# Optimization experiments

Hardware: AMD Instinct MI355X
Metric: run time of the kernel (lower is better)

## Reference

```python
import jax, jax.numpy as jnp
import numpy as np

D_MODEL = 1024
HEADS = 16
HEAD_DIM = D_MODEL // HEADS
SEQ_LEN = 2048
BATCH = 2
LN_EPS = 1e-5


def _layernorm(x, gamma, beta):
    mu = jnp.mean(x, axis=-1, keepdims=True)
    var = jnp.var(x, axis=-1, keepdims=True)
    return (x - mu) * jax.lax.rsqrt(var + LN_EPS) * gamma + beta


def setup_inputs() -> dict:
    key = jax.random.key(0)
    ks = jax.random.split(key, 12)
    d, h = D_MODEL, 4 * D_MODEL
    s = lambda fan_in: 1.0 / np.sqrt(fan_in)
    return {
        "x": jax.random.normal(ks[0], (BATCH, SEQ_LEN, d), dtype=jnp.float32),
        "W_qkv": jax.random.uniform(ks[1], (d, 3 * d), minval=-s(d), maxval=s(d)),
        "b_qkv": jax.random.uniform(ks[2], (3 * d,), minval=-s(d), maxval=s(d)),
        "W1": jax.random.uniform(ks[3], (d, h), minval=-s(d), maxval=s(d)),
        "b1": jax.random.uniform(ks[4], (h,), minval=-s(d), maxval=s(d)),
        "W2": jax.random.uniform(ks[5], (h, d), minval=-s(h), maxval=s(h)),
        "b2": jax.random.uniform(ks[6], (d,), minval=-s(h), maxval=s(h)),
        "ln1_g": jnp.ones((d,), jnp.float32),
        "ln1_b": jnp.zeros((d,), jnp.float32),
        "ln2_g": jnp.ones((d,), jnp.float32),
        "ln2_b": jnp.zeros((d,), jnp.float32),
    }


def reference(x, W_qkv, b_qkv, W1, b1, W2, b2, ln1_g, ln1_b, ln2_g, ln2_b):
    B, T, C = x.shape
    # QKV projection -> [B, T, 3, H, hs] -> q,k,v each [B, H, T, hs]
    qkv = (x @ W_qkv + b_qkv).reshape(B, T, 3, HEADS, HEAD_DIM)
    qkv = jnp.transpose(qkv, (2, 0, 3, 1, 4))
    q, k, v = qkv[0], qkv[1], qkv[2]
    # Naive causal attention with full [B,H,T,T] score matrix (matches source)
    A = jnp.einsum("bhqd,bhkd->bhqk", q, k) / jnp.sqrt(jnp.float32(HEAD_DIM))
    causal = jnp.tril(jnp.ones((T, T), dtype=bool))
    A = jnp.where(causal, A, -jnp.inf)
    A = jax.nn.softmax(A, axis=-1)
    attn = jnp.einsum("bhqk,bhkd->bhqd", A, v)  # [B,H,T,hs]
    attn = jnp.transpose(attn, (0, 2, 1, 3)).reshape(B, T, C)
    # Residual + LN, FFN, residual + LN (dropout=0 / eval)
    h = _layernorm(x + attn, ln1_g, ln1_b)
    ff = jax.nn.relu(h @ W1 + b1) @ W2 + b2
    return _layernorm(h + ff, ln2_g, ln2_b)
```

## Files before the change

kernel.cpp:

```cpp
#include <hip/hip_runtime.h>

#define D_MODEL 1024
#define HEADS   16
#define HEAD_DIM 64
#define SEQ     2048
#define BATCH   2
#define ROWS    (BATCH*SEQ)
#define FFDIM   4096

typedef __attribute__((ext_vector_type(8))) short short8;
typedef __attribute__((ext_vector_type(4))) float f32x4;
typedef __attribute__((ext_vector_type(4))) unsigned short us4;

typedef const __attribute__((address_space(1))) unsigned int* gptr_t;
typedef __attribute__((address_space(3))) unsigned int* lptr_t;

__device__ __forceinline__ unsigned short f2bf(float f){
  unsigned int x = __float_as_uint(f);
  x += 0x7fffu + ((x >> 16) & 1u);
  return (unsigned short)(x >> 16);
}

__device__ __forceinline__ float wave_sum(float x){
  #pragma unroll
  for (int off = 32; off; off >>= 1) x += __shfl_xor(x, off);
  return x;
}

__global__ __launch_bounds__(256) void cast_bf16_kernel(const float* __restrict__ in,
                                                        unsigned short* __restrict__ out, int n4){
  int i = blockIdx.x * 256 + threadIdx.x;
  if (i >= n4) return;
  float4 v = *(const float4*)(in + (size_t)i * 4);
  us4 o;
  o[0] = f2bf(v.x); o[1] = f2bf(v.y); o[2] = f2bf(v.z); o[3] = f2bf(v.w);
  *(us4*)(out + (size_t)i * 4) = o;
}

__global__ __launch_bounds__(256) void transpose_cast_kernel(const float* __restrict__ in,
                                                             unsigned short* __restrict__ out,
                                                             int R, int C){
  __shared__ float tile[32][33];
  const int bc = blockIdx.x * 32, br = blockIdx.y * 32;
  const int tx = threadIdx.x & 31, ty = threadIdx.x >> 5;
  #pragma unroll
  for (int j = 0; j < 4; ++j)
    tile[ty + 8*j][tx] = in[(size_t)(br + ty + 8*j) * C + bc + tx];
  __syncthreads();
  #pragma unroll
  for (int j = 0; j < 4; ++j)
    out[(size_t)(bc + ty + 8*j) * R + br + tx] = f2bf(tile[tx][ty + 8*j]);
}

template<int EPI>
__global__ __launch_bounds__(256) void gemm_kernel(const unsigned short* __restrict__ A,
                                                   const unsigned short* __restrict__ BT,
                                                   const float* __restrict__ bias,
                                                   int M, int N, int K, int kchunk,
                                                   int gx, int gy,
                                                   float* __restrict__ outF,
                                                   unsigned short* __restrict__ qo,
                                                   unsigned short* __restrict__ ko,
                                                   unsigned short* __restrict__ vT){
  __shared__ __align__(16) unsigned short Alds[2][128 * 32];
  __shared__ __align__(16) unsigned short Blds[2][128 * 32];
  const int tid = threadIdx.x;
  const int lane = tid & 63;
  const int wid = tid >> 6;
  const int wr = wid >> 1, wc = wid & 1;
  const int lrow = lane & 15, lgrp = lane >> 4;

  const int nwg = gridDim.x;
  const int cpx = nwg >> 3;
  const int wg = (blockIdx.x & 7) * cpx + (blockIdx.x >> 3);
  const int nx = wg % gx;
  const int rest = wg / gx;
  const int my = rest % gy;
  const int sk = rest / gy;

  const int m0 = my * 128, n0 = nx * 128;
  const int kbase0 = sk * kchunk;
  const int sr = lane >> 2, sc = (lane & 3) * 8;

  f32x4 acc[4][4];
  #pragma unroll
  for (int i = 0; i < 4; ++i)
    #pragma unroll
    for (int j = 0; j < 4; ++j)
      acc[i][j] = f32x4{0.f, 0.f, 0.f, 0.f};

  #pragma unroll
  for (int it = 0; it < 2; ++it){
    const int c = wid * 2 + it;
    const int r = c * 16 + sr;
    __builtin_amdgcn_global_load_lds(
        (gptr_t)(const void*)(A + (size_t)(m0 + r) * K + kbase0 + sc),
        (lptr_t)(void*)(&Alds[0][c * 512]), 16, 0, 0);
    __builtin_amdgcn_global_load_lds(
        (gptr_t)(const void*)(BT + (size_t)(n0 + r) * K + kbase0 + sc),
        (lptr_t)(void*)(&Blds[0][c * 512]), 16, 0, 0);
  }

  const int nk = kchunk >> 5;
  int cur = 0;
  for (int kt = 0; kt < nk; ++kt){
    __syncthreads();
    if (kt + 1 < nk){
      const int kb = kbase0 + (kt + 1) * 32;
      #pragma unroll
      for (int it = 0; it < 2; ++it){
        const int c = wid * 2 + it;
        const int r = c * 16 + sr;
        __builtin_amdgcn_global_load_lds(
            (gptr_t)(const void*)(A + (size_t)(m0 + r) * K + kb + sc),
            (lptr_t)(void*)(&Alds[cur ^ 1][c * 512]), 16, 0, 0);
        __builtin_amdgcn_global_load_lds(
            (gptr_t)(const void*)(BT + (size_t)(n0 + r) * K + kb + sc),
            (lptr_t)(void*)(&Blds[cur ^ 1][c * 512]), 16, 0, 0);
      }
    }
    short8 af[4], bfr[4];
    #pragma unroll
    for (int f = 0; f < 4; ++f){
      af[f]  = *(const short8*)&Alds[cur][(wr * 64 + f * 16 + lrow) * 32 + lgrp * 8];
      bfr[f] = *(const short8*)&Blds[cur][(wc * 64 + f * 16 + lrow) * 32 + lgrp * 8];
    }
    __builtin_amdgcn_s_setprio(1);
    #pragma unroll
    for (int i = 0; i < 4; ++i)
      #pragma unroll
      for (int j = 0; j < 4; ++j)
        acc[i][j] = __builtin_amdgcn_mfma_f32_16x16x32_bf16(af[i], bfr[j], acc[i][j], 0, 0, 0);
    __builtin_amdgcn_s_setprio(0);
    cur ^= 1;
  }

  #pragma unroll
  for (int i = 0; i < 4; ++i){
    const int rg = m0 + wr * 64 + i * 16 + lgrp * 4;
    #pragma unroll
    for (int j = 0; j < 4; ++j){
      const int cg = n0 + wc * 64 + j * 16 + lrow;
      if constexpr (EPI == 0){
        const float bb = bias[cg];
        const int which = cg >> 10, rem = cg & 1023;
        const int hh = rem >> 6, dd = rem & 63;
        const int bb_ = rg >> 11, tt = rg & 2047;
        const size_t bh = (size_t)(bb_ * HEADS + hh);
        if (which == 2){
          us4 pk;
          #pragma unroll
          for (int r = 0; r < 4; ++r) pk[r] = f2bf(acc[i][j][r] + bb);
          *(us4*)(vT + (bh * 64 + dd) * SEQ + tt) = pk;
        } else {
          unsigned short* dst = which ? ko : qo;
          const float sc2 = which ? 1.0f : 0.18033688f;
          #pragma unroll
          for (int r = 0; r < 4; ++r)
            dst[(bh * SEQ + tt + r) * 64 + dd] = f2bf((acc[i][j][r] + bb) * sc2);
        }
      } else {
        float* outP = outF + (size_t)sk * M * N;
        #pragma unroll
        for (int r = 0; r < 4; ++r)
          outP[(size_t)(rg + r) * N + cg] = acc[i][j][r];
      }
    }
  }
}

template<int EPI>
__global__ __launch_bounds__(512, 1) void gemm2h_kernel(const unsigned short* __restrict__ A,
                                                        const unsigned short* __restrict__ BT,
                                                        const float* __restrict__ bias,
                                                        int M, int N, int K, int kchunk,
                                                        int gx, int gy,
                                                        unsigned short* __restrict__ outH){
  __shared__ __align__(16) unsigned short Ab[2][2][256 * 32];
  __shared__ __align__(16) unsigned short Bb[2][2][256 * 32];
  const int tid = threadIdx.x, lane = tid & 63, wid = tid >> 6;
  const int wm = wid >> 2, wn = wid & 3;
  const int lr = lane & 15, g = lane >> 4;

  const int nwg = gridDim.x, cpx = nwg >> 3;
  const int wg = (blockIdx.x & 7) * cpx + (blockIdx.x >> 3);
  const int nx = wg % gx;
  const int rest = wg / gx;
  const int my = rest % gy;
  const int sk = rest / gy;
  const int m0 = my * 256, n0 = nx * 256, kb0 = sk * kchunk;
  const int nk = kchunk >> 6;

  f32x4 acc[8][4];
  #pragma unroll
  for (int i = 0; i < 8; ++i)
    #pragma unroll
    for (int j = 0; j < 4; ++j)
      acc[i][j] = f32x4{0.f, 0.f, 0.f, 0.f};

  auto STAGE = [&](int op, int t, int kh){
    const int d_ = t & 1;
    unsigned short* base = op ? &Bb[d_][kh][0] : &Ab[d_][kh][0];
    const unsigned short* src = op ? BT : A;
    const int r0 = op ? n0 : m0;
    #pragma unroll
    for (int j = 0; j < 2; ++j){
      const int L = tid + j * 512;
      const int row = L >> 2, c = L & 3;
      __builtin_amdgcn_global_load_lds(
          (gptr_t)(const void*)(src + (size_t)(r0 + row) * K + kb0 + t * 64 + kh * 32
                                + ((c ^ ((row >> 1) & 3)) << 3)),
          (lptr_t)(void*)(base + L * 8), 16, 0, 0);
    }
  };

  short8 afA[8], bfA[4], afB[8], bfB[4];

  #define READS(da, db, d_, kh_)                                                          \
    _Pragma("unroll")                                                                     \
    for (int i = 0; i < 8; ++i){                                                          \
      const int row = wm * 128 + i * 16 + lr;                                             \
      da[i] = *(const short8*)&Ab[d_][kh_][row * 32 + ((g ^ ((row >> 1) & 3)) << 3)];     \
    }                                                                                     \
    _Pragma("unroll")                                                                     \
    for (int j = 0; j < 4; ++j){                                                          \
      const int row = wn * 64 + j * 16 + lr;                                              \
      db[j] = *(const short8*)&Bb[d_][kh_][row * 32 + ((g ^ ((row >> 1) & 3)) << 3)];     \
    }

  #define MFMA32(sa, sb)                                                                  \
    _Pragma("unroll")                                                                     \
    for (int i = 0; i < 8; ++i)                                                           \
      _Pragma("unroll")                                                                   \
      for (int j = 0; j < 4; ++j)                                                         \
        acc[i][j] = __builtin_amdgcn_mfma_f32_16x16x32_bf16(sa[i], sb[j], acc[i][j], 0, 0, 0);

  STAGE(0,0,0); STAGE(1,0,0); STAGE(0,0,1); STAGE(1,0,1);
  if (nk > 1){ STAGE(0,1,0); STAGE(1,1,0); }
  if (nk > 1) asm volatile("s_waitcnt vmcnt(8)" ::: "memory");
  else        asm volatile("s_waitcnt vmcnt(4)" ::: "memory");
  __builtin_amdgcn_s_barrier();
  READS(afA, bfA, 0, 0)

  for (int t = 0; t < nk; ++t){
    const int d = t & 1, dn = d ^ 1;

    if (t + 1 < nk) asm volatile("s_waitcnt vmcnt(4)" ::: "memory");
    else            asm volatile("s_waitcnt vmcnt(0)" ::: "memory");
    __builtin_amdgcn_s_barrier();
    if (t + 1 < nk){ STAGE(0, t + 1, 1); STAGE(1, t + 1, 1); }
    READS(afB, bfB, d, 1)
    asm volatile("s_waitcnt lgkmcnt(12)" ::: "memory");
    __builtin_amdgcn_sched_barrier(0);
    __builtin_amdgcn_s_setprio(1);
    MFMA32(afA, bfA)
    __builtin_amdgcn_s_setprio(0);

    if (t + 1 < nk) asm volatile("s_waitcnt vmcnt(4)" ::: "memory");
    else            asm volatile("s_waitcnt vmcnt(0)" ::: "memory");
    __builtin_amdgcn_s_barrier();
    if (t + 2 < nk){ STAGE(0, t + 2, 0); STAGE(1, t + 2, 0); }
    if (t + 1 < nk){
      READS(afA, bfA, dn, 0)
      asm volatile("s_waitcnt lgkmcnt(12)" ::: "memory");
    } else {
      asm volatile("s_waitcnt lgkmcnt(0)" ::: "memory");
    }
    __builtin_amdgcn_sched_barrier(0);
    __builtin_amdgcn_s_setprio(1);
    MFMA32(afB, bfB)
    __builtin_amdgcn_s_setprio(0);
  }
  #undef READS
  #undef MFMA32

  #pragma unroll
  for (int i = 0; i < 8; ++i){
    const int rg = m0 + wm * 128 + i * 16 + g * 4;
    #pragma unroll
    for (int j = 0; j < 4; ++j){
      const int cg = n0 + wn * 64 + j * 16 + lr;
      if constexpr (EPI == 1){
        const float bb = bias[cg];
        #pragma unroll
        for (int r = 0; r < 4; ++r)
          outH[(size_t)(rg + r) * N + cg] = f2bf(fmaxf(acc[i][j][r] + bb, 0.f));
      } else {
        unsigned short* dst = outH + (size_t)sk * M * N;
        #pragma unroll
        for (int r = 0; r < 4; ++r)
          dst[(size_t)(rg + r) * N + cg] = f2bf(acc[i][j][r]);
      }
    }
  }
}

__global__ __launch_bounds__(256) void attn_mfma_kernel(const unsigned short* __restrict__ Qb,
                                                        const unsigned short* __restrict__ Kb,
                                                        const unsigned short* __restrict__ VT,
                                                        float* __restrict__ Op){
  __shared__ __align__(16) char Kl[2][8192];
  __shared__ __align__(16) char Vl[2][8192];
  __shared__ __align__(16) char Pl[4][4096];
  const int tid = threadIdx.x;
  const int w = tid >> 6, lane = tid & 63;
  const int lr = lane & 15, g = lane >> 4;

  const int bx = blockIdx.x, u = bx & 255, half = bx >> 8;
  const int g8 = u >> 5;
  const int qg = half ? g8 : 15 - g8;
  const int bh = u & 31;

  const int q0w = qg * 128 + w * 32;
  const int qA = q0w + lr, qB = qA + 16;

  const char* const KbB = (const char*)(Kb + (size_t)bh * SEQ * 64);
  const char* const VbB = (const char*)(VT + (size_t)bh * 64 * SEQ);
  char* const PbA = Pl[w];
  char* const PbB = Pl[w] + 2048;

  const unsigned short* qra = Qb + ((size_t)bh * SEQ + qA) * 64 + g * 8;
  const short8 qfA0 = *(const short8*)(qra);
  const short8 qfA1 = *(const short8*)(qra + 32);
  const short8 qfB0 = *(const short8*)(qra + 16 * 64);
  const short8 qfB1 = *(const short8*)(qra + 16 * 64 + 32);

  f32x4 oA[4], oB[4];
  #pragma unroll
  for (int dt = 0; dt < 4; ++dt){ oA[dt] = f32x4{0.f,0.f,0.f,0.f}; oB[dt] = f32x4{0.f,0.f,0.f,0.f}; }
  float lA = 0.f, lB = 0.f;
  const int swzl = (lr & 7) << 4;

  const int kbmax = 2 * qg + 1;

  short8 st[4];
  {
    #pragma unroll
    for (int c = 0; c < 2; ++c){
      const int L = c * 4096 + tid * 16;
      st[c] = *(const short8*)(KbB + L);
      const int row = L >> 7, col = L & 127;
      st[2 + c] = *(const short8*)(VbB + (size_t)row * 4096 + col);
    }
  }

  for (int kb = 0; kb <= kbmax; ++kb){
    const int p = kb & 1;
    const int k0 = kb * 64;

    #pragma unroll
    for (int c = 0; c < 2; ++c){
      const int L = c * 4096 + tid * 16;
      const int row = L >> 7, col = L & 127;
      const int dst = row * 128 + (col ^ ((row & 7) << 4));
      *(short8*)(Kl[p] + dst) = st[c];
      *(short8*)(Vl[p] + dst) = st[2 + c];
    }
    __syncthreads();

    if (kb < kbmax){
      #pragma unroll
      for (int c = 0; c < 2; ++c){
        const int L = c * 4096 + tid * 16;
        st[c] = *(const short8*)(KbB + (size_t)(kb + 1) * 8192 + L);
        const int row = L >> 7, col = L & 127;
        st[2 + c] = *(const short8*)(VbB + (size_t)row * 4096 + (size_t)(kb + 1) * 128 + col);
      }
    }

    f32x4 sA[4], sB[4];
    __builtin_amdgcn_s_setprio(1);
    #pragma unroll
    for (int kt = 0; kt < 4; ++kt){
      const int row = kt * 16 + lr;
      const int ro = row * 128, sw = (row & 7) << 4;
      const short8 kf0 = *(const short8*)(Kl[p] + ro + ((g * 16) ^ sw));
      const short8 kf1 = *(const short8*)(Kl[p] + ro + ((64 + g * 16) ^ sw));
      sA[kt] = __builtin_amdgcn_mfma_f32_16x16x32_bf16(kf0, qfA0, f32x4{0.f,0.f,0.f,0.f}, 0, 0, 0);
      sA[kt] = __builtin_amdgcn_mfma_f32_16x16x32_bf16(kf1, qfA1, sA[kt], 0, 0, 0);
      sB[kt] = __builtin_amdgcn_mfma_f32_16x16x32_bf16(kf0, qfB0, f32x4{0.f,0.f,0.f,0.f}, 0, 0, 0);
      sB[kt] = __builtin_amdgcn_mfma_f32_16x16x32_bf16(kf1, qfB1, sB[kt], 0, 0, 0);
    }
    __builtin_amdgcn_s_setprio(0);

    if (kb >= kbmax - 1){
      #pragma unroll
      for (int kt = 0; kt < 4; ++kt)
        #pragma unroll
        for (int r = 0; r < 4; ++r){
          const int key = k0 + kt * 16 + g * 4 + r;
          if (key > qA) sA[kt][r] = -INFINITY;
          if (key > qB) sB[kt][r] = -INFINITY;
        }
    }

    {
      float sum = 0.f;
      #pragma unroll
      for (int kt = 0; kt < 4; ++kt){
        #pragma unroll
        for (int r = 0; r < 4; ++r){
          const float pp = __builtin_amdgcn_exp2f(sA[kt][r]);
          sA[kt][r] = pp; sum += pp;
        }
        unsigned int p01, p23;
        asm("v_cvt_pk_bf16_f32 %0, %1, %2" : "=v"(p01) : "v"(sA[kt][0]), "v"(sA[kt][1]));
        asm("v_cvt_pk_bf16_f32 %0, %1, %2" : "=v"(p23) : "v"(sA[kt][2]), "v"(sA[kt][3]));
        uint2 pk; pk.x = p01; pk.y = p23;
        *(uint2*)(PbA + lr * 128 + ((kt * 32 + g * 8) ^ swzl)) = pk;
      }
      sum += __shfl_xor(sum, 16);
      sum += __shfl_xor(sum, 32);
      lA += sum;
    }
    {
      float sum = 0.f;
      #pragma unroll
      for (int kt = 0; kt < 4; ++kt){
        #pragma unroll
        for (int r = 0; r < 4; ++r){
          const float pp = __builtin_amdgcn_exp2f(sB[kt][r]);
          sB[kt][r] = pp; sum += pp;
        }
        unsigned int p01, p23;
        asm("v_cvt_pk_bf16_f32 %0, %1, %2" : "=v"(p01) : "v"(sB[kt][0]), "v"(sB[kt][1]));
        asm("v_cvt_pk_bf16_f32 %0, %1, %2" : "=v"(p23) : "v"(sB[kt][2]), "v"(sB[kt][3]));
        uint2 pk; pk.x = p01; pk.y = p23;
        *(uint2*)(PbB + lr * 128 + ((kt * 32 + g * 8) ^ swzl)) = pk;
      }
      sum += __shfl_xor(sum, 16);
      sum += __shfl_xor(sum, 32);
      lB += sum;
    }

    const short8 paA0 = *(const short8*)(PbA + lr * 128 + ((g * 16) ^ swzl));
    const short8 paA1 = *(const short8*)(PbA + lr * 128 + ((64 + g * 16) ^ swzl));
    const short8 paB0 = *(const short8*)(PbB + lr * 128 + ((g * 16) ^ swzl));
    const short8 paB1 = *(const short8*)(PbB + lr * 128 + ((64 + g * 16) ^ swzl));
    __builtin_amdgcn_s_setprio(1);
    #pragma unroll
    for (int dt = 0; dt < 4; ++dt){
      const int row = dt * 16 + lr;
      const int ro = row * 128, sw = (row & 7) << 4;
      const short8 vf0 = *(const short8*)(Vl[p] + ro + ((g * 16) ^ sw));
      const short8 vf1 = *(const short8*)(Vl[p] + ro + ((64 + g * 16) ^ sw));
      oA[dt] = __builtin_amdgcn_mfma_f32_16x16x32_bf16(paA0, vf0, oA[dt], 0, 0, 0);
      oA[dt] = __builtin_amdgcn_mfma_f32_16x16x32_bf16(paA1, vf1, oA[dt], 0, 0, 0);
      oB[dt] = __builtin_amdgcn_mfma_f32_16x16x32_bf16(paB0, vf0, oB[dt], 0, 0, 0);
      oB[dt] = __builtin_amdgcn_mfma_f32_16x16x32_bf16(paB1, vf1, oB[dt], 0, 0, 0);
    }
    __builtin_amdgcn_s_setprio(0);
  }

  const int b = bh >> 4, hh = bh & 15;
  {
    float lv[4];
    #pragma unroll
    for (int r = 0; r < 4; ++r) lv[r] = __shfl(lA, g * 4 + r);
    #pragma unroll
    for (int dt = 0; dt < 4; ++dt)
      #pragma unroll
      for (int r = 0; r < 4; ++r)
        Op[((size_t)(b * SEQ) + q0w + g * 4 + r) * D_MODEL + hh * 64 + dt * 16 + lr] = oA[dt][r] / lv[r];
  }
  {
    float lv[4];
    #pragma unroll
    for (int r = 0; r < 4; ++r) lv[r] = __shfl(lB, g * 4 + r);
    #pragma unroll
    for (int dt = 0; dt < 4; ++dt)
      #pragma unroll
      for (int r = 0; r < 4; ++r)
        Op[((size_t)(b * SEQ) + q0w + 16 + g * 4 + r) * D_MODEL + hh * 64 + dt * 16 + lr] = oB[dt][r] / lv[r];
  }
}

__global__ __launch_bounds__(256) void ln_kernel(const float* __restrict__ A,
                                                 const float* __restrict__ B1,
                                                 const unsigned short* __restrict__ P4,
                                                 size_t pstride,
                                                 const float* __restrict__ bias,
                                                 const float* __restrict__ g,
                                                 const float* __restrict__ be,
                                                 float* __restrict__ outF,
                                                 unsigned short* __restrict__ outH){
  const int row = blockIdx.x, tid = threadIdx.x;
  const size_t base = (size_t)row * D_MODEL + tid * 4;
  float4 va = *(const float4*)(A + base);
  float v0 = va.x, v1 = va.y, v2 = va.z, v3 = va.w;
  if (B1){
    float4 vb = *(const float4*)(B1 + base);
    v0 += vb.x; v1 += vb.y; v2 += vb.z; v3 += vb.w;
  }
  if (P4){
    #pragma unroll
    for (int p = 0; p < 4; ++p){
      us4 u = *(const us4*)(P4 + p * pstride + base);
      v0 += __uint_as_float((unsigned int)u[0] << 16);
      v1 += __uint_as_float((unsigned int)u[1] << 16);
      v2 += __uint_as_float((unsigned int)u[2] << 16);
      v3 += __uint_as_float((unsigned int)u[3] << 16);
    }
  }
  if (bias){
    float4 vd = *(const float4*)(bias + tid * 4);
    v0 += vd.x; v1 += vd.y; v2 += vd.z; v3 += vd.w;
  }
  float s  = v0 + v1 + v2 + v3;
  float ss = v0*v0 + v1*v1 + v2*v2 + v3*v3;
  s = wave_sum(s); ss = wave_sum(ss);
  __shared__ float red[8];
  const int w = tid >> 6, lane = tid & 63;
  if (!lane){ red[w] = s; red[4 + w] = ss; }
  __syncthreads();
  s  = red[0] + red[1] + red[2] + red[3];
  ss = red[4] + red[5] + red[6] + red[7];
  const float mu  = s * (1.0f / D_MODEL);
  const float var = ss * (1.0f / D_MODEL) - mu * mu;
  const float rstd = rsqrtf(var + 1e-5f);
  float4 gg = *(const float4*)(g  + tid * 4);
  float4 bb = *(const float4*)(be + tid * 4);
  const float r0 = (v0 - mu) * rstd * gg.x + bb.x;
  const float r1 = (v1 - mu) * rstd * gg.y + bb.y;
  const float r2 = (v2 - mu) * rstd * gg.z + bb.z;
  const float r3 = (v3 - mu) * rstd * gg.w + bb.w;
  float4 of; of.x = r0; of.y = r1; of.z = r2; of.w = r3;
  *(float4*)(outF + base) = of;
  if (outH){
    us4 oh; oh[0] = f2bf(r0); oh[1] = f2bf(r1); oh[2] = f2bf(r2); oh[3] = f2bf(r3);
    *(us4*)(outH + base) = oh;
  }
}

__global__ __launch_bounds__(256) void ln2f_kernel(const float* __restrict__ A,
                                                   const float* __restrict__ B1,
                                                   const float* __restrict__ bias,
                                                   const float* __restrict__ g,
                                                   const float* __restrict__ be,
                                                   float* __restrict__ outF){
  const int row = blockIdx.x, tid = threadIdx.x;
  const size_t base = (size_t)row * D_MODEL + tid * 4;
  float4 va = *(const float4*)(A + base);
  float4 vb = *(const float4*)(B1 + base);
  float4 vd = *(const float4*)(bias + tid * 4);
  float v0 = va.x + vb.x + vd.x, v1 = va.y + vb.y + vd.y;
  float v2 = va.z + vb.z + vd.z, v3 = va.w + vb.w + vd.w;
  float s  = v0 + v1 + v2 + v3;
  float ss = v0*v0 + v1*v1 + v2*v2 + v3*v3;
  s = wave_sum(s); ss = wave_sum(ss);
  __shared__ float red[8];
  const int w = tid >> 6, lane = tid & 63;
  if (!lane){ red[w] = s; red[4 + w] = ss; }
  __syncthreads();
  s  = red[0] + red[1] + red[2] + red[3];
  ss = red[4] + red[5] + red[6] + red[7];
  const float mu  = s * (1.0f / D_MODEL);
  const float var = ss * (1.0f / D_MODEL) - mu * mu;
  const float rstd = rsqrtf(var + 1e-5f);
  float4 gg = *(const float4*)(g  + tid * 4);
  float4 bb = *(const float4*)(be + tid * 4);
  float4 of;
  of.x = (v0 - mu) * rstd * gg.x + bb.x;
  of.y = (v1 - mu) * rstd * gg.y + bb.y;
  of.z = (v2 - mu) * rstd * gg.z + bb.z;
  of.w = (v3 - mu) * rstd * gg.w + bb.w;
  *(float4*)(outF + base) = of;
}

extern "C" void kernel_launch(void* const* d_in, const int* in_sizes, int n_in,
                              void* d_out, int out_size, void* d_ws, size_t ws_size,
                              hipStream_t stream){
  (void)in_sizes; (void)n_in; (void)out_size;
  const float* x     = (const float*)d_in[0];
  const float* W_qkv = (const float*)d_in[1];
  const float* b_qkv = (const float*)d_in[2];
  const float* W1    = (const float*)d_in[3];
  const float* b1    = (const float*)d_in[4];
  const float* W2    = (const float*)d_in[5];
  const float* b2    = (const float*)d_in[6];
  const float* ln1g  = (const float*)d_in[7];
  const float* ln1b  = (const float*)d_in[8];
  const float* ln2g  = (const float*)d_in[9];
  const float* ln2b  = (const float*)d_in[10];

  char* ws = (char*)d_ws;
  const size_t MB = 1024ull * 1024ull;
  unsigned short* WqkvT = (unsigned short*)(ws + 0 * MB);
  unsigned short* W1T   = (unsigned short*)(ws + 6 * MB);
  unsigned short* W2T   = (unsigned short*)(ws + 14 * MB);
  unsigned short* xbf   = (unsigned short*)(ws + 22 * MB);
  unsigned short* qB    = (unsigned short*)(ws + 30 * MB);
  unsigned short* kB    = (unsigned short*)(ws + 39 * MB);
  unsigned short* vT    = (unsigned short*)(ws + 48 * MB);
  float* attn = (float*)(ws + 57 * MB);
  float* hF           = (float*)(ws + 30 * MB);
  unsigned short* hB  = (unsigned short*)(ws + 46 * MB);
  unsigned short* ff1 = (unsigned short*)(ws + 54 * MB);
  unsigned short* pbf = (unsigned short*)(ws + 86 * MB);
  float* p0           = (float*)(ws + 86 * MB);

  const int use2h = (ws_size >= 118 * MB);

  cast_bf16_kernel<<<4096, 256, 0, stream>>>(x, xbf, ROWS * D_MODEL / 4);
  transpose_cast_kernel<<<dim3(96, 32), 256, 0, stream>>>(W_qkv, WqkvT, 1024, 3072);
  transpose_cast_kernel<<<dim3(128, 32), 256, 0, stream>>>(W1, W1T, 1024, 4096);
  transpose_cast_kernel<<<dim3(32, 128), 256, 0, stream>>>(W2, W2T, 4096, 1024);

  gemm_kernel<0><<<768, 256, 0, stream>>>(
      xbf, WqkvT, b_qkv, ROWS, 3072, 1024, 1024, 24, 32, nullptr, qB, kB, vT);

  attn_mfma_kernel<<<512, 256, 0, stream>>>(qB, kB, vT, attn);

  ln_kernel<<<ROWS, 256, 0, stream>>>(x, attn, nullptr, 0, nullptr, ln1g, ln1b, hF, hB);

  gemm2h_kernel<1><<<256, 512, 0, stream>>>(
      hB, W1T, b1, ROWS, FFDIM, 1024, 1024, 16, 16, ff1);

  if (use2h){
    gemm2h_kernel<4><<<256, 512, 0, stream>>>(
        ff1, W2T, nullptr, ROWS, 1024, FFDIM, 1024, 4, 16, pbf);
    ln_kernel<<<ROWS, 256, 0, stream>>>(hF, nullptr, pbf, (size_t)ROWS * 1024, b2,
                                        ln2g, ln2b, (float*)d_out, nullptr);
  } else {
    gemm_kernel<3><<<256, 256, 0, stream>>>(
        ff1, W2T, nullptr, ROWS, 1024, FFDIM, FFDIM, 8, 32, p0, nullptr, nullptr, nullptr);
    ln2f_kernel<<<ROWS, 256, 0, stream>>>(hF, p0, b2, ln2g, ln2b, (float*)d_out);
  }
}
```

Before: 215.1 us.

## Simplify GEMM LDS pipeline to single fragment set; drop fp32 LN1 output

The 256x256 bf16 GEMM previously double-buffered register fragments, overlapping the LDS reads for the next K-half with the MFMAs of the current one. It now uses one fragment set: each half waits for its reads to finish (lgkmcnt(0)) before issuing MFMAs, which lowers register pressure but gives up that read/MFMA overlap. Separately, LN1 no longer writes an fp32 copy of h, and LN2 reads the bf16 h as its residual, cutting memory traffic. This drops precision on the second residual path.

```diff
diff --git a/kernel.cpp b/kernel.cpp
--- a/kernel.cpp
+++ b/kernel.cpp
@@ -19,6 +19,9 @@
   unsigned int x = __float_as_uint(f);
   x += 0x7fffu + ((x >> 16) & 1u);
   return (unsigned short)(x >> 16);
+}
+__device__ __forceinline__ float bf2f(unsigned short u){
+  return __uint_as_float((unsigned int)u << 16);
 }
 
 __device__ __forceinline__ float wave_sum(float x){
@@ -170,7 +173,7 @@
 }
 
 template<int EPI>
-__global__ __launch_bounds__(512, 1) void gemm2h_kernel(const unsigned short* __restrict__ A,
+__global__ __launch_bounds__(512, 1) void gemm4b_kernel(const unsigned short* __restrict__ A,
                                                         const unsigned short* __restrict__ BT,
                                                         const float* __restrict__ bias,
                                                         int M, int N, int K, int kchunk,
@@ -214,62 +217,52 @@
     }
   };
 
-  short8 afA[8], bfA[4], afB[8], bfB[4];
-
-  #define READS(da, db, d_, kh_)                                                          \
+  short8 afr[8], bfr[4];
+
+  #define READS(d_, kh_)                                                                  \
     _Pragma("unroll")                                                                     \
     for (int i = 0; i < 8; ++i){                                                          \
       const int row = wm * 128 + i * 16 + lr;                                             \
-      da[i] = *(const short8*)&Ab[d_][kh_][row * 32 + ((g ^ ((row >> 1) & 3)) << 3)];     \
+      afr[i] = *(const short8*)&Ab[d_][kh_][row * 32 + ((g ^ ((row >> 1) & 3)) << 3)];    \
     }                                                                                     \
     _Pragma("unroll")                                                                     \
     for (int j = 0; j < 4; ++j){                                                          \
       const int row = wn * 64 + j * 16 + lr;                                              \
-      db[j] = *(const short8*)&Bb[d_][kh_][row * 32 + ((g ^ ((row >> 1) & 3)) << 3)];     \
-    }
-
-  #define MFMA32(sa, sb)                                                                  \
+      bfr[j] = *(const short8*)&Bb[d_][kh_][row * 32 + ((g ^ ((row >> 1) & 3)) << 3)];    \
+    }
+
+  #define MFMA32()                                                                        \
+    __builtin_amdgcn_sched_barrier(0);                                                    \
+    __builtin_amdgcn_s_setprio(1);                                                        \
     _Pragma("unroll")                                                                     \
     for (int i = 0; i < 8; ++i)                                                           \
       _Pragma("unroll")                                                                   \
       for (int j = 0; j < 4; ++j)                                                         \
-        acc[i][j] = __builtin_amdgcn_mfma_f32_16x16x32_bf16(sa[i], sb[j], acc[i][j], 0, 0, 0);
+        acc[i][j] = __builtin_amdgcn_mfma_f32_16x16x32_bf16(afr[i], bfr[j], acc[i][j], 0, 0, 0); \
+    __builtin_amdgcn_s_setprio(0);
 
   STAGE(0,0,0); STAGE(1,0,0); STAGE(0,0,1); STAGE(1,0,1);
   if (nk > 1){ STAGE(0,1,0); STAGE(1,1,0); }
-  if (nk > 1) asm volatile("s_waitcnt vmcnt(8)" ::: "memory");
-  else        asm volatile("s_waitcnt vmcnt(4)" ::: "memory");
-  __builtin_amdgcn_s_barrier();
-  READS(afA, bfA, 0, 0)
 
   for (int t = 0; t < nk; ++t){
     const int d = t & 1, dn = d ^ 1;
 
-    if (t + 1 < nk) asm volatile("s_waitcnt vmcnt(4)" ::: "memory");
+    if (t + 1 < nk) asm volatile("s_waitcnt vmcnt(8)" ::: "memory");
+    else            asm volatile("s_waitcnt vmcnt(4)" ::: "memory");
+    __builtin_amdgcn_s_barrier();
+    READS(d, 0)
+    if (t + 1 < nk){ STAGE(0, t + 1, 1); STAGE(1, t + 1, 1); }
+    asm volatile("s_waitcnt lgkmcnt(0)" ::: "memory");
+    MFMA32()
+
+    if (t + 1 < nk) asm volatile("s_waitcnt vmcnt(8)" ::: "memory");
     else            asm volatile("s_waitcnt vmcnt(0)" ::: "memory");
     __builtin_amdgcn_s_barrier();
-    if (t + 1 < nk){ STAGE(0, t + 1, 1); STAGE(1, t + 1, 1); }
-    READS(afB, bfB, d, 1)
-    asm volatile("s_waitcnt lgkmcnt(12)" ::: "memory");
-    __builtin_amdgcn_sched_barrier(0);
-    __builtin_amdgcn_s_setprio(1);
-    MFMA32(afA, bfA)
-    __builtin_amdgcn_s_setprio(0);
-
-    if (t + 1 < nk) asm volatile("s_waitcnt vmcnt(4)" ::: "memory");
-    else            asm volatile("s_waitcnt vmcnt(0)" ::: "memory");
-    __builtin_amdgcn_s_barrier();
+    READS(d, 1)
     if (t + 2 < nk){ STAGE(0, t + 2, 0); STAGE(1, t + 2, 0); }
-    if (t + 1 < nk){
-      READS(afA, bfA, dn, 0)
-      asm volatile("s_waitcnt lgkmcnt(12)" ::: "memory");
-    } else {
-      asm volatile("s_waitcnt lgkmcnt(0)" ::: "memory");
-    }
-    __builtin_amdgcn_sched_barrier(0);
-    __builtin_amdgcn_s_setprio(1);
-    MFMA32(afB, bfB)
-    __builtin_amdgcn_s_setprio(0);
+    asm volatile("s_waitcnt lgkmcnt(0)" ::: "memory");
+    MFMA32()
+    (void)dn;
   }
   #undef READS
   #undef MFMA32
@@ -475,7 +468,8 @@
   }
 }
 
-__global__ __launch_bounds__(256) void ln_kernel(const float* __restrict__ A,
+__global__ __launch_bounds__(256) void ln_kernel(const float* __restrict__ Af32,
+                                                 const unsigned short* __restrict__ Abf,
                                                  const float* __restrict__ B1,
                                                  const unsigned short* __restrict__ P4,
                                                  size_t pstride,
@@ -486,8 +480,14 @@
                                                  unsigned short* __restrict__ outH){
   const int row = blockIdx.x, tid = threadIdx.x;
   const size_t base = (size_t)row * D_MODEL + tid * 4;
-  float4 va = *(const float4*)(A + base);
-  float v0 = va.x, v1 = va.y, v2 = va.z, v3 = va.w;
+  float v0, v1, v2, v3;
+  if (Af32){
+    float4 va = *(const float4*)(Af32 + base);
+    v0 = va.x; v1 = va.y; v2 = va.z; v3 = va.w;
+  } else {
+    us4 ua = *(const us4*)(Abf + base);
+    v0 = bf2f(ua[0]); v1 = bf2f(ua[1]); v2 = bf2f(ua[2]); v3 = bf2f(ua[3]);
+  }
   if (B1){
     float4 vb = *(const float4*)(B1 + base);
     v0 += vb.x; v1 += vb.y; v2 += vb.z; v3 += vb.w;
@@ -496,10 +496,7 @@
     #pragma unroll
     for (int p = 0; p < 4; ++p){
       us4 u = *(const us4*)(P4 + p * pstride + base);
-      v0 += __uint_as_float((unsigned int)u[0] << 16);
-      v1 += __uint_as_float((unsigned int)u[1] << 16);
-      v2 += __uint_as_float((unsigned int)u[2] << 16);
-      v3 += __uint_as_float((unsigned int)u[3] << 16);
+      v0 += bf2f(u[0]); v1 += bf2f(u[1]); v2 += bf2f(u[2]); v3 += bf2f(u[3]);
     }
   }
   if (bias){
@@ -524,47 +521,14 @@
   const float r1 = (v1 - mu) * rstd * gg.y + bb.y;
   const float r2 = (v2 - mu) * rstd * gg.z + bb.z;
   const float r3 = (v3 - mu) * rstd * gg.w + bb.w;
-  float4 of; of.x = r0; of.y = r1; of.z = r2; of.w = r3;
-  *(float4*)(outF + base) = of;
+  if (outF){
+    float4 of; of.x = r0; of.y = r1; of.z = r2; of.w = r3;
+    *(float4*)(outF + base) = of;
+  }
   if (outH){
     us4 oh; oh[0] = f2bf(r0); oh[1] = f2bf(r1); oh[2] = f2bf(r2); oh[3] = f2bf(r3);
     *(us4*)(outH + base) = oh;
   }
-}
-
-__global__ __launch_bounds__(256) void ln2f_kernel(const float* __restrict__ A,
-                                                   const float* __restrict__ B1,
-                                                   const float* __restrict__ bias,
-                                                   const float* __restrict__ g,
-                                                   const float* __restrict__ be,
-                                                   float* __restrict__ outF){
-  const int row = blockIdx.x, tid = threadIdx.x;
-  const size_t base = (size_t)row * D_MODEL + tid * 4;
-  float4 va = *(const float4*)(A + base);
-  float4 vb = *(const float4*)(B1 + base);
-  float4 vd = *(const float4*)(bias + tid * 4);
-  float v0 = va.x + vb.x + vd.x, v1 = va.y + vb.y + vd.y;
-  float v2 = va.z + vb.z + vd.z, v3 = va.w + vb.w + vd.w;
-  float s  = v0 + v1 + v2 + v3;
-  float ss = v0*v0 + v1*v1 + v2*v2 + v3*v3;
-  s = wave_sum(s); ss = wave_sum(ss);
-  __shared__ float red[8];
-  const int w = tid >> 6, lane = tid & 63;
-  if (!lane){ red[w] = s; red[4 + w] = ss; }
-  __syncthreads();
-  s  = red[0] + red[1] + red[2] + red[3];
-  ss = red[4] + red[5] + red[6] + red[7];
-  const float mu  = s * (1.0f / D_MODEL);
-  const float var = ss * (1.0f / D_MODEL) - mu * mu;
-  const float rstd = rsqrtf(var + 1e-5f);
-  float4 gg = *(const float4*)(g  + tid * 4);
-  float4 bb = *(const float4*)(be + tid * 4);
-  float4 of;
-  of.x = (v0 - mu) * rstd * gg.x + bb.x;
-  of.y = (v1 - mu) * rstd * gg.y + bb.y;
-  of.z = (v2 - mu) * rstd * gg.z + bb.z;
-  of.w = (v3 - mu) * rstd * gg.w + bb.w;
-  *(float4*)(outF + base) = of;
 }
 
 extern "C" void kernel_launch(void* const* d_in, const int* in_sizes, int n_in,
@@ -593,13 +557,12 @@
   unsigned short* kB    = (unsigned short*)(ws + 39 * MB);
   unsigned short* vT    = (unsigned short*)(ws + 48 * MB);
   float* attn = (float*)(ws + 57 * MB);
-  float* hF           = (float*)(ws + 30 * MB);
   unsigned short* hB  = (unsigned short*)(ws + 46 * MB);
   unsigned short* ff1 = (unsigned short*)(ws + 54 * MB);
   unsigned short* pbf = (unsigned short*)(ws + 86 * MB);
   float* p0           = (float*)(ws + 86 * MB);
 
-  const int use2h = (ws_size >= 118 * MB);
+  const int use4b = (ws_size >= 118 * MB);
 
   cast_bf16_kernel<<<4096, 256, 0, stream>>>(x, xbf, ROWS * D_MODEL / 4);
   transpose_cast_kernel<<<dim3(96, 32), 256, 0, stream>>>(W_qkv, WqkvT, 1024, 3072);
@@ -611,19 +574,21 @@
 
   attn_mfma_kernel<<<512, 256, 0, stream>>>(qB, kB, vT, attn);
 
-  ln_kernel<<<ROWS, 256, 0, stream>>>(x, attn, nullptr, 0, nullptr, ln1g, ln1b, hF, hB);
-
-  gemm2h_kernel<1><<<256, 512, 0, stream>>>(
+  ln_kernel<<<ROWS, 256, 0, stream>>>(x, nullptr, attn, nullptr, 0, nullptr,
+                                      ln1g, ln1b, nullptr, hB);
+
+  gemm4b_kernel<1><<<256, 512, 0, stream>>>(
       hB, W1T, b1, ROWS, FFDIM, 1024, 1024, 16, 16, ff1);
 
-  if (use2h){
-    gemm2h_kernel<4><<<256, 512, 0, stream>>>(
+  if (use4b){
+    gemm4b_kernel<4><<<256, 512, 0, stream>>>(
         ff1, W2T, nullptr, ROWS, 1024, FFDIM, 1024, 4, 16, pbf);
-    ln_kernel<<<ROWS, 256, 0, stream>>>(hF, nullptr, pbf, (size_t)ROWS * 1024, b2,
+    ln_kernel<<<ROWS, 256, 0, stream>>>(nullptr, hB, nullptr, pbf, (size_t)ROWS * 1024, b2,
                                         ln2g, ln2b, (float*)d_out, nullptr);
   } else {
     gemm_kernel<3><<<256, 256, 0, stream>>>(
         ff1, W2T, nullptr, ROWS, 1024, FFDIM, FFDIM, 8, 32, p0, nullptr, nullptr, nullptr);
-    ln2f_kernel<<<ROWS, 256, 0, stream>>>(hF, p0, b2, ln2g, ln2b, (float*)d_out);
-  }
-}
+    ln_kernel<<<ROWS, 256, 0, stream>>>(nullptr, hB, p0, nullptr, 0, b2,
+                                        ln2g, ln2b, (float*)d_out, nullptr);
+  }
+}
```

Result: faster. 196.6 us (-8.6%).
